# Kernel tuning notes

Measured on AMD Instinct MI355X. Metric: run time of the kernel, lower is better.

## Reference

```python
import jax, jax.numpy as jnp
import numpy as np

KMIX = 16
N_CH = 302   # hardcoded number of output channels in MDNLayer
N_POS = 394  # hardcoded evaluation grid size


def setup_inputs() -> dict:
    key = jax.random.key(0)
    k1, k2 = jax.random.split(key)
    B, D = 32, 1024
    units = N_CH * KMIX * 3  # 14496
    x = jax.random.normal(k1, (B, D), dtype=jnp.float32)
    # 'random_normal' keras initializer uses stddev=0.05
    w = jax.random.normal(k2, (D, units), dtype=jnp.float32) * 0.05
    b = jnp.zeros((units,), dtype=jnp.float32)
    return {"x": x, "w": w, "b": b}


def reference(x, w, b):
    B = x.shape[0]
    # Dense projection then reshape to (B, 3*KMIX, 302) as in the original
    y = (x @ w + b).reshape(B, 3 * KMIX, N_CH)
    mu = y[:, 0 * KMIX:1 * KMIX, :]   # (B, K, 302)
    sig = y[:, 1 * KMIX:2 * KMIX, :]  # (B, K, 302) used raw as Normal scale
    pi = y[:, 2 * KMIX:3 * KMIX, :]   # (B, K, 302) mixture logits

    pos = jnp.linspace(0.0, 1.0, N_POS, dtype=x.dtype)  # (394,)
    inv_sqrt_2pi = jnp.asarray(1.0 / np.sqrt(2.0 * np.pi), dtype=x.dtype)

    # Per-component Normal pdf at each grid point: (B, K, 302, 394)
    z = (pos[None, None, None, :] - mu[..., None]) / sig[..., None]
    comp_pdf = jnp.exp(-0.5 * z * z) * (inv_sqrt_2pi / sig[..., None])

    # Mixture weights: softmax over the K components (axis=1)
    weights = jax.nn.softmax(pi, axis=1)  # (B, K, 302)

    # Weighted sum over components -> (B, 302, 394)
    res = jnp.einsum('bkc,bkcp->bcp', weights, comp_pdf)
    return res[..., None]  # (B, 302, 394, 1)
```

## Files before the change

kernel.cpp:

```cpp
#include <hip/hip_runtime.h>

#define BATCH 32
#define DIM 1024
#define NCH 302
#define KMIX 16
#define UNITS 14496
#define NPOS 394
#define KSPLIT 8
#define KCHUNK (DIM / KSPLIT)
#define NTILE 256
#define NTILES ((UNITS + NTILE - 1) / NTILE)
#define BSUB 8

__global__ __launch_bounds__(256) void gemm_kernel(
    const float* __restrict__ x, const float* __restrict__ w,
    float* __restrict__ partial)
{
  __shared__ float xs[BATCH][KCHUNK];
  const int tid = threadIdx.x;
  const int k0  = blockIdx.y * KCHUNK;
  const int n0  = blockIdx.x * NTILE;

#pragma unroll
  for (int j = 0; j < 4; ++j) {
    const int idx4 = tid + j * 256;
    const int b    = idx4 >> 5;
    const int d4   = idx4 & 31;
    const float4 v = *(const float4*)(x + b * DIM + k0 + d4 * 4);
    *(float4*)(&xs[b][d4 * 4]) = v;
  }
  __syncthreads();

  const int lane = tid & 63;
  const int bg   = tid >> 6;
  const bool st  = (n0 + lane * 4) < UNITS;
  int nc = n0 + lane * 4;
  if (nc > UNITS - 4) nc = UNITS - 4;

  float4 acc[BSUB];
#pragma unroll
  for (int bi = 0; bi < BSUB; ++bi) acc[bi] = make_float4(0.f, 0.f, 0.f, 0.f);

  const float* wp = w + (size_t)k0 * UNITS + nc;
  float4 wv[4], wn[4];
#pragma unroll
  for (int j = 0; j < 4; ++j) wv[j] = *(const float4*)(wp + (size_t)j * UNITS);

  for (int dd = 0; dd < KCHUNK; dd += 4) {
    if (dd + 4 < KCHUNK) {
#pragma unroll
      for (int j = 0; j < 4; ++j)
        wn[j] = *(const float4*)(wp + (size_t)(dd + 4 + j) * UNITS);
    }
#pragma unroll
    for (int bi = 0; bi < BSUB; ++bi) {
      const float4 xv = *(const float4*)(&xs[bg * BSUB + bi][dd]);
      acc[bi].x = fmaf(xv.x, wv[0].x, acc[bi].x);
      acc[bi].y = fmaf(xv.x, wv[0].y, acc[bi].y);
      acc[bi].z = fmaf(xv.x, wv[0].z, acc[bi].z);
      acc[bi].w = fmaf(xv.x, wv[0].w, acc[bi].w);
      acc[bi].x = fmaf(xv.y, wv[1].x, acc[bi].x);
      acc[bi].y = fmaf(xv.y, wv[1].y, acc[bi].y);
      acc[bi].z = fmaf(xv.y, wv[1].z, acc[bi].z);
      acc[bi].w = fmaf(xv.y, wv[1].w, acc[bi].w);
      acc[bi].x = fmaf(xv.z, wv[2].x, acc[bi].x);
      acc[bi].y = fmaf(xv.z, wv[2].y, acc[bi].y);
      acc[bi].z = fmaf(xv.z, wv[2].z, acc[bi].z);
      acc[bi].w = fmaf(xv.z, wv[2].w, acc[bi].w);
      acc[bi].x = fmaf(xv.w, wv[3].x, acc[bi].x);
      acc[bi].y = fmaf(xv.w, wv[3].y, acc[bi].y);
      acc[bi].z = fmaf(xv.w, wv[3].z, acc[bi].z);
      acc[bi].w = fmaf(xv.w, wv[3].w, acc[bi].w);
    }
#pragma unroll
    for (int j = 0; j < 4; ++j) wv[j] = wn[j];
  }

  if (st) {
    float* pp = partial + ((size_t)blockIdx.y * BATCH + bg * BSUB) * UNITS + nc;
#pragma unroll
    for (int bi = 0; bi < BSUB; ++bi)
      *(float4*)(pp + (size_t)bi * UNITS) = acc[bi];
  }
}

__global__ __launch_bounds__(256) void reduce_kernel(
    const float* __restrict__ partial, const float* __restrict__ bias,
    float* __restrict__ y)
{
  const int f4   = blockIdx.x * 256 + threadIdx.x;
  const int base = f4 * 4;
  float4 s = make_float4(0.f, 0.f, 0.f, 0.f);
#pragma unroll
  for (int k = 0; k < KSPLIT; ++k) {
    const float4 v = *(const float4*)(partial + (size_t)k * (BATCH * UNITS) + base);
    s.x += v.x; s.y += v.y; s.z += v.z; s.w += v.w;
  }
  const int n = base % UNITS;
  const float4 bv = *(const float4*)(bias + n);
  s.x += bv.x; s.y += bv.y; s.z += bv.z; s.w += bv.w;
  *(float4*)(y + base) = s;
}

__global__ __launch_bounds__(256) void mdn_kernel(
    const float* __restrict__ y, float* __restrict__ out)
{
  const int lane = threadIdx.x & 63;
  int pair = blockIdx.x * 4 + (threadIdx.x >> 6);
  pair = __builtin_amdgcn_readfirstlane(pair);
  const int b = pair / NCH;
  const int c = pair - b * NCH;
  const float* yb = y + b * UNITS + c;

  float pw[KMIX];
  float m = -3.4e38f;
#pragma unroll
  for (int k = 0; k < KMIX; ++k) {
    pw[k] = yb[(2 * KMIX + k) * NCH];
    m = fmaxf(m, pw[k]);
  }
  float ssum = 0.0f;
#pragma unroll
  for (int k = 0; k < KMIX; ++k) { pw[k] = __expf(pw[k] - m); ssum += pw[k]; }
  const float wnorm = 0.39894228040143267f / ssum;

  float posv[7];
#pragma unroll
  for (int i = 0; i < 7; ++i)
    posv[i] = (float)(lane + i * 64) * (1.0f / (NPOS - 1));

  float acc[7] = {0.f, 0.f, 0.f, 0.f, 0.f, 0.f, 0.f};
#pragma unroll
  for (int k = 0; k < KMIX; ++k) {
    const float mu   = yb[k * NCH];
    const float sig  = yb[(KMIX + k) * NCH];
    const float isig = 1.0f / sig;
    const float coef = pw[k] * wnorm * isig;
    const float nmu  = -mu * isig;
#pragma unroll
    for (int i = 0; i < 7; ++i) {
      const float t = fmaf(posv[i], isig, nmu);
      acc[i] = fmaf(coef, exp2f(t * t * -0.72134752044448170f), acc[i]);
    }
  }

  float* op = out + (size_t)pair * NPOS;
#pragma unroll
  for (int i = 0; i < 7; ++i) {
    const int p = lane + i * 64;
    if (p < NPOS) op[p] = acc[i];
  }
}

extern "C" void kernel_launch(void* const* d_in, const int* in_sizes, int n_in,
                              void* d_out, int out_size, void* d_ws, size_t ws_size,
                              hipStream_t stream) {
  const float* x    = (const float*)d_in[0];
  const float* w    = (const float*)d_in[1];
  const float* bias = (const float*)d_in[2];
  float* out     = (float*)d_out;
  float* partial = (float*)d_out;
  float* y       = (float*)d_ws;

  gemm_kernel<<<dim3(NTILES, KSPLIT), 256, 0, stream>>>(x, w, partial);
  reduce_kernel<<<(BATCH * UNITS / 4) / 256, 256, 0, stream>>>(partial, bias, y);
  mdn_kernel<<<(BATCH * NCH) / 4, 256, 0, stream>>>(y, out);
}
```

Before: 152.3 us.

## Double split-K, flatten GEMM grid, transpose reduced output for MDN staging

The split-K factor goes from 8 to 16 and the GEMM grid is flattened to 1D, giving more blocks to fill the GPU. The weight prefetch is now two-stage, using two register sets of 4 rows each per 8-step iteration. The reduce kernel writes y transposed into a per-(batch, channel) layout of 48 contiguous values. The MDN kernel then stages these into shared memory instead of doing strided global loads. Partials move from the output buffer into workspace, which doubles partial traffic and assumes a workspace of at least 32 MB plus the transposed buffer.

```diff
diff --git a/kernel.cpp b/kernel.cpp
--- a/kernel.cpp
+++ b/kernel.cpp
@@ -6,11 +6,12 @@
 #define KMIX 16
 #define UNITS 14496
 #define NPOS 394
-#define KSPLIT 8
+#define KSPLIT 16
 #define KCHUNK (DIM / KSPLIT)
 #define NTILE 256
-#define NTILES ((UNITS + NTILE - 1) / NTILE)
+#define NTILES 57
 #define BSUB 8
+#define NPAIRS (BATCH * NCH)
 
 __global__ __launch_bounds__(256) void gemm_kernel(
     const float* __restrict__ x, const float* __restrict__ w,
@@ -18,16 +19,17 @@
 {
   __shared__ float xs[BATCH][KCHUNK];
   const int tid = threadIdx.x;
-  const int k0  = blockIdx.y * KCHUNK;
-  const int n0  = blockIdx.x * NTILE;
-
-#pragma unroll
-  for (int j = 0; j < 4; ++j) {
+  const int kch = blockIdx.x / NTILES;
+  const int tile = blockIdx.x - kch * NTILES;
+  const int k0  = kch * KCHUNK;
+  const int n0  = tile * NTILE;
+
+#pragma unroll
+  for (int j = 0; j < 2; ++j) {
     const int idx4 = tid + j * 256;
-    const int b    = idx4 >> 5;
-    const int d4   = idx4 & 31;
-    const float4 v = *(const float4*)(x + b * DIM + k0 + d4 * 4);
-    *(float4*)(&xs[b][d4 * 4]) = v;
+    const int b    = idx4 >> 4;
+    const int d4   = idx4 & 15;
+    *(float4*)(&xs[b][d4 * 4]) = *(const float4*)(x + b * DIM + k0 + d4 * 4);
   }
   __syncthreads();
 
@@ -42,42 +44,73 @@
   for (int bi = 0; bi < BSUB; ++bi) acc[bi] = make_float4(0.f, 0.f, 0.f, 0.f);
 
   const float* wp = w + (size_t)k0 * UNITS + nc;
-  float4 wv[4], wn[4];
-#pragma unroll
-  for (int j = 0; j < 4; ++j) wv[j] = *(const float4*)(wp + (size_t)j * UNITS);
-
-  for (int dd = 0; dd < KCHUNK; dd += 4) {
-    if (dd + 4 < KCHUNK) {
+  float4 wa[4], wb[4];
+#pragma unroll
+  for (int j = 0; j < 4; ++j) wa[j] = *(const float4*)(wp + (size_t)j * UNITS);
+#pragma unroll
+  for (int j = 0; j < 4; ++j) wb[j] = *(const float4*)(wp + (size_t)(4 + j) * UNITS);
+
+  for (int dd = 0; dd < KCHUNK; dd += 8) {
+    const int nx = dd + 8;
+    float4 wa2[4], wb2[4];
+    if (nx < KCHUNK) {
 #pragma unroll
       for (int j = 0; j < 4; ++j)
-        wn[j] = *(const float4*)(wp + (size_t)(dd + 4 + j) * UNITS);
+        wa2[j] = *(const float4*)(wp + (size_t)(nx + j) * UNITS);
     }
 #pragma unroll
     for (int bi = 0; bi < BSUB; ++bi) {
       const float4 xv = *(const float4*)(&xs[bg * BSUB + bi][dd]);
-      acc[bi].x = fmaf(xv.x, wv[0].x, acc[bi].x);
-      acc[bi].y = fmaf(xv.x, wv[0].y, acc[bi].y);
-      acc[bi].z = fmaf(xv.x, wv[0].z, acc[bi].z);
-      acc[bi].w = fmaf(xv.x, wv[0].w, acc[bi].w);
-      acc[bi].x = fmaf(xv.y, wv[1].x, acc[bi].x);
-      acc[bi].y = fmaf(xv.y, wv[1].y, acc[bi].y);
-      acc[bi].z = fmaf(xv.y, wv[1].z, acc[bi].z);
-      acc[bi].w = fmaf(xv.y, wv[1].w, acc[bi].w);
-      acc[bi].x = fmaf(xv.z, wv[2].x, acc[bi].x);
-      acc[bi].y = fmaf(xv.z, wv[2].y, acc[bi].y);
-      acc[bi].z = fmaf(xv.z, wv[2].z, acc[bi].z);
-      acc[bi].w = fmaf(xv.z, wv[2].w, acc[bi].w);
-      acc[bi].x = fmaf(xv.w, wv[3].x, acc[bi].x);
-      acc[bi].y = fmaf(xv.w, wv[3].y, acc[bi].y);
-      acc[bi].z = fmaf(xv.w, wv[3].z, acc[bi].z);
-      acc[bi].w = fmaf(xv.w, wv[3].w, acc[bi].w);
-    }
-#pragma unroll
-    for (int j = 0; j < 4; ++j) wv[j] = wn[j];
+      acc[bi].x = fmaf(xv.x, wa[0].x, acc[bi].x);
+      acc[bi].y = fmaf(xv.x, wa[0].y, acc[bi].y);
+      acc[bi].z = fmaf(xv.x, wa[0].z, acc[bi].z);
+      acc[bi].w = fmaf(xv.x, wa[0].w, acc[bi].w);
+      acc[bi].x = fmaf(xv.y, wa[1].x, acc[bi].x);
+      acc[bi].y = fmaf(xv.y, wa[1].y, acc[bi].y);
+      acc[bi].z = fmaf(xv.y, wa[1].z, acc[bi].z);
+      acc[bi].w = fmaf(xv.y, wa[1].w, acc[bi].w);
+      acc[bi].x = fmaf(xv.z, wa[2].x, acc[bi].x);
+      acc[bi].y = fmaf(xv.z, wa[2].y, acc[bi].y);
+      acc[bi].z = fmaf(xv.z, wa[2].z, acc[bi].z);
+      acc[bi].w = fmaf(xv.z, wa[2].w, acc[bi].w);
+      acc[bi].x = fmaf(xv.w, wa[3].x, acc[bi].x);
+      acc[bi].y = fmaf(xv.w, wa[3].y, acc[bi].y);
+      acc[bi].z = fmaf(xv.w, wa[3].z, acc[bi].z);
+      acc[bi].w = fmaf(xv.w, wa[3].w, acc[bi].w);
+    }
+    if (nx < KCHUNK) {
+#pragma unroll
+      for (int j = 0; j < 4; ++j)
+        wb2[j] = *(const float4*)(wp + (size_t)(nx + 4 + j) * UNITS);
+    }
+#pragma unroll
+    for (int bi = 0; bi < BSUB; ++bi) {
+      const float4 xv = *(const float4*)(&xs[bg * BSUB + bi][dd + 4]);
+      acc[bi].x = fmaf(xv.x, wb[0].x, acc[bi].x);
+      acc[bi].y = fmaf(xv.x, wb[0].y, acc[bi].y);
+      acc[bi].z = fmaf(xv.x, wb[0].z, acc[bi].z);
+      acc[bi].w = fmaf(xv.x, wb[0].w, acc[bi].w);
+      acc[bi].x = fmaf(xv.y, wb[1].x, acc[bi].x);
+      acc[bi].y = fmaf(xv.y, wb[1].y, acc[bi].y);
+      acc[bi].z = fmaf(xv.y, wb[1].z, acc[bi].z);
+      acc[bi].w = fmaf(xv.y, wb[1].w, acc[bi].w);
+      acc[bi].x = fmaf(xv.z, wb[2].x, acc[bi].x);
+      acc[bi].y = fmaf(xv.z, wb[2].y, acc[bi].y);
+      acc[bi].z = fmaf(xv.z, wb[2].z, acc[bi].z);
+      acc[bi].w = fmaf(xv.z, wb[2].w, acc[bi].w);
+      acc[bi].x = fmaf(xv.w, wb[3].x, acc[bi].x);
+      acc[bi].y = fmaf(xv.w, wb[3].y, acc[bi].y);
+      acc[bi].z = fmaf(xv.w, wb[3].z, acc[bi].z);
+      acc[bi].w = fmaf(xv.w, wb[3].w, acc[bi].w);
+    }
+    if (nx < KCHUNK) {
+#pragma unroll
+      for (int j = 0; j < 4; ++j) { wa[j] = wa2[j]; wb[j] = wb2[j]; }
+    }
   }
 
   if (st) {
-    float* pp = partial + ((size_t)blockIdx.y * BATCH + bg * BSUB) * UNITS + nc;
+    float* pp = partial + ((size_t)kch * BATCH + bg * BSUB) * UNITS + nc;
 #pragma unroll
     for (int bi = 0; bi < BSUB; ++bi)
       *(float4*)(pp + (size_t)bi * UNITS) = acc[bi];
@@ -86,37 +119,50 @@
 
 __global__ __launch_bounds__(256) void reduce_kernel(
     const float* __restrict__ partial, const float* __restrict__ bias,
-    float* __restrict__ y)
+    float* __restrict__ yt)
 {
-  const int f4   = blockIdx.x * 256 + threadIdx.x;
-  const int base = f4 * 4;
-  float4 s = make_float4(0.f, 0.f, 0.f, 0.f);
+  const int idx  = blockIdx.x * 256 + threadIdx.x;
+  const int base = idx * 4;
+  float4 s4 = make_float4(0.f, 0.f, 0.f, 0.f);
 #pragma unroll
   for (int k = 0; k < KSPLIT; ++k) {
     const float4 v = *(const float4*)(partial + (size_t)k * (BATCH * UNITS) + base);
-    s.x += v.x; s.y += v.y; s.z += v.z; s.w += v.w;
-  }
-  const int n = base % UNITS;
+    s4.x += v.x; s4.y += v.y; s4.z += v.z; s4.w += v.w;
+  }
+  const int b = base / UNITS;
+  const int n = base - b * UNITS;
   const float4 bv = *(const float4*)(bias + n);
-  s.x += bv.x; s.y += bv.y; s.z += bv.z; s.w += bv.w;
-  *(float4*)(y + base) = s;
+  s4.x += bv.x; s4.y += bv.y; s4.z += bv.z; s4.w += bv.w;
+
+  float vs[4] = {s4.x, s4.y, s4.z, s4.w};
+#pragma unroll
+  for (int j = 0; j < 4; ++j) {
+    const int nj = n + j;
+    const int s  = nj / NCH;
+    const int c  = nj - s * NCH;
+    yt[((size_t)b * NCH + c) * 48 + s] = vs[j];
+  }
 }
 
 __global__ __launch_bounds__(256) void mdn_kernel(
-    const float* __restrict__ y, float* __restrict__ out)
+    const float* __restrict__ yt, float* __restrict__ out)
 {
-  const int lane = threadIdx.x & 63;
-  int pair = blockIdx.x * 4 + (threadIdx.x >> 6);
-  pair = __builtin_amdgcn_readfirstlane(pair);
-  const int b = pair / NCH;
-  const int c = pair - b * NCH;
-  const float* yb = y + b * UNITS + c;
+  __shared__ float ps[4][48];
+  const int tid  = threadIdx.x;
+  const int lane = tid & 63;
+  const int bg   = tid >> 6;
+
+  if (tid < 192) ps[tid / 48][tid % 48] = yt[(size_t)blockIdx.x * 192 + tid];
+  __syncthreads();
+
+  const int pair = blockIdx.x * 4 + bg;
+  const float* pp = ps[bg];
 
   float pw[KMIX];
   float m = -3.4e38f;
 #pragma unroll
   for (int k = 0; k < KMIX; ++k) {
-    pw[k] = yb[(2 * KMIX + k) * NCH];
+    pw[k] = pp[32 + k];
     m = fmaxf(m, pw[k]);
   }
   float ssum = 0.0f;
@@ -132,8 +178,8 @@
   float acc[7] = {0.f, 0.f, 0.f, 0.f, 0.f, 0.f, 0.f};
 #pragma unroll
   for (int k = 0; k < KMIX; ++k) {
-    const float mu   = yb[k * NCH];
-    const float sig  = yb[(KMIX + k) * NCH];
+    const float mu   = pp[k];
+    const float sig  = pp[16 + k];
     const float isig = 1.0f / sig;
     const float coef = pw[k] * wnorm * isig;
     const float nmu  = -mu * isig;
@@ -159,10 +205,10 @@
   const float* w    = (const float*)d_in[1];
   const float* bias = (const float*)d_in[2];
   float* out     = (float*)d_out;
-  float* partial = (float*)d_out;
-  float* y       = (float*)d_ws;
-
-  gemm_kernel<<<dim3(NTILES, KSPLIT), 256, 0, stream>>>(x, w, partial);
-  reduce_kernel<<<(BATCH * UNITS / 4) / 256, 256, 0, stream>>>(partial, bias, y);
-  mdn_kernel<<<(BATCH * NCH) / 4, 256, 0, stream>>>(y, out);
-}
+  float* partial = (float*)d_ws;
+  float* yt      = (float*)((char*)d_ws + (size_t)32 * 1024 * 1024);
+
+  gemm_kernel<<<NTILES * KSPLIT, 256, 0, stream>>>(x, w, partial);
+  reduce_kernel<<<(BATCH * UNITS / 4) / 256, 256, 0, stream>>>(partial, bias, yt);
+  mdn_kernel<<<NPAIRS / 4, 256, 0, stream>>>(yt, out);
+}
```

Result: faster. 143.6 us (-5.7%).
